# Kernel optimization log

Hardware: AMD Instinct MI355X
Metric: run time of the kernel (lower is better)

## Reference

```python
import jax, jax.numpy as jnp
import numpy as np

TOKENS, IN_F, OUT_F, R = 8192, 4096, 4096, 16
NS_STEPS = 5
NS_EPS = 1e-7


def newtonschulz5(G, steps=NS_STEPS, eps=NS_EPS):
    # Quintic Newton-Schulz orthogonalization: sigma -> 1, preserving U, V.
    a, b, c = 3.4445, -4.775, 2.0315
    X = G / (jnp.linalg.norm(G) + eps)
    transposed = G.shape[0] > G.shape[1]
    if transposed:
        X = X.T
    for _ in range(steps):
        A = X @ X.T                 # [m, m]
        B = b * A + c * (A @ A)
        X = a * X + B @ X
    if transposed:
        X = X.T
    return X


def setup_inputs() -> dict:
    key = jax.random.key(0)
    kx, kw, kb, ka, kbb = jax.random.split(key, 5)
    x = jax.random.normal(kx, (TOKENS, IN_F), dtype=jnp.float32)
    # base linear params
    W = jax.random.normal(kw, (OUT_F, IN_F), dtype=jnp.float32) / np.sqrt(IN_F)
    bias = jax.random.normal(kb, (OUT_F,), dtype=jnp.float32) * 0.01
    # LoRA params: A ~ orthogonal-ish rows, B small (init_scale/sqrt(out*r))
    lora_A = jax.random.normal(ka, (R, IN_F), dtype=jnp.float32) / np.sqrt(IN_F)
    init_std = 0.01 / np.sqrt(OUT_F * R)
    lora_B = jax.random.normal(kbb, (OUT_F, R), dtype=jnp.float32) * init_std
    return {"x": x, "W": W, "bias": bias, "lora_A": lora_A, "lora_B": lora_B}


def reference(x, W, bias, lora_A, lora_B):
    # base_out = x @ W^T + bias
    base_out = x @ W.T + bias
    # G = B A  (full [out, in] materialization, as in the original)
    G = lora_B @ lora_A
    alpha = jnp.linalg.norm(G)
    M = newtonschulz5(G)
    # lora_dropout = 0 -> identity
    lora_out = x @ M.T
    return base_out + alpha * lora_out
```

## Files before the change

### kernel.cpp

```cpp
#include <hip/hip_runtime.h>
#include <hip/hip_bf16.h>
#include <math.h>

#define TOKENS 8192
#define IN_F   4096
#define OUT_F  4096
#define LR     16

typedef __bf16 bf16_t;
typedef __attribute__((ext_vector_type(8)))  __bf16 bf16x8;
typedef __attribute__((ext_vector_type(4)))  __bf16 bf16x4;
typedef __attribute__((ext_vector_type(4)))  float  floatx4;
typedef __attribute__((ext_vector_type(16))) float  floatx16;

#define GL2LDS(gp, lp) \
    __builtin_amdgcn_global_load_lds((const __attribute__((address_space(1))) unsigned int*)(gp), \
                                     (__attribute__((address_space(3))) unsigned int*)(lp), 16, 0, 0)

__global__ void pq_kernel(const float* __restrict__ A, const float* __restrict__ B,
                          float* __restrict__ P, float* __restrict__ Q) {
    __shared__ float red[256];
    const int b = blockIdx.x, t = threadIdx.x;
    float s = 0.f;
    if (b < 256) {
        const int i = b >> 4, j = b & 15;
        const float* ai = A + (size_t)i * IN_F;
        const float* aj = A + (size_t)j * IN_F;
        for (int k = t; k < IN_F; k += 256) s += ai[k] * aj[k];
    } else {
        const int i = (b - 256) >> 4, j = (b - 256) & 15;
        for (int k = t; k < OUT_F; k += 256) s += B[k * LR + i] * B[k * LR + j];
    }
    red[t] = s; __syncthreads();
    for (int off = 128; off > 0; off >>= 1) {
        if (t < off) red[t] += red[t + off];
        __syncthreads();
    }
    if (t == 0) {
        if (b < 256) P[b] = red[0];
        else         Q[b - 256] = red[0];
    }
}

__global__ void ns_kernel(const float* __restrict__ P, const float* __restrict__ Q,
                          float* __restrict__ Sc) {
    __shared__ double Ps[256], Qs[256], Ss[256], Ys[256], Zs[256], Ts[256], Us[256], Vs[256];
    __shared__ double alpha_s, inv_n;
    const int t = threadIdx.x, i = t >> 4, j = t & 15;
    Ps[t] = P[t]; Qs[t] = Q[t];
    __syncthreads();
    if (t == 0) {
        double s = 0.0;
        for (int a = 0; a < 16; ++a)
            for (int b2 = 0; b2 < 16; ++b2) s += Ps[a * 16 + b2] * Qs[b2 * 16 + a];
        const double al = sqrt(s);
        alpha_s = al;
        inv_n   = 1.0 / (al + 1e-7);
    }
    __syncthreads();
    Ss[t] = (i == j) ? inv_n : 0.0;
    __syncthreads();
    const double ca = 3.4445, cb = -4.775, cc = 2.0315;
    for (int step = 0; step < 5; ++step) {
        double s;
        s = 0; for (int q = 0; q < 16; ++q) s += Ss[i*16+q] * Ps[q*16+j]; Ys[t] = s; __syncthreads();
        s = 0; for (int q = 0; q < 16; ++q) s += Ys[i*16+q] * Ss[j*16+q]; Zs[t] = s; __syncthreads();
        s = 0; for (int q = 0; q < 16; ++q) s += Zs[i*16+q] * Qs[q*16+j]; Ts[t] = s; __syncthreads();
        s = 0; for (int q = 0; q < 16; ++q) s += Ts[i*16+q] * Ss[q*16+j]; Us[t] = s; __syncthreads();
        s = 0; for (int q = 0; q < 16; ++q) s += Ts[i*16+q] * Us[q*16+j]; Vs[t] = s; __syncthreads();
        Ss[t] = ca * Ss[t] + cb * Us[t] + cc * Vs[t];
        __syncthreads();
    }
    Sc[t] = (float)(alpha_s * Ss[t]);
}

__global__ void sca_kernel(const float* __restrict__ Sc, const float* __restrict__ A,
                           float* __restrict__ ScA) {
    const int idx = blockIdx.x * 256 + threadIdx.x;
    const int r = idx >> 12, i = idx & 4095;
    float s = 0.f;
    for (int q = 0; q < 16; ++q) s += Sc[r * 16 + q] * A[q * IN_F + i];
    ScA[r * IN_F + i] = s;
}

__global__ void weff_kernel(const float* __restrict__ W, const float* __restrict__ Bm,
                            const float* __restrict__ ScA, bf16_t* __restrict__ Wb) {
    const int b = blockIdx.x, t = threadIdx.x;
    const int o0 = (b >> 2) * 4;
    const int i  = (b & 3) * 1024 + t * 4;
    float4 acc[4];
    #pragma unroll
    for (int r = 0; r < 4; ++r) acc[r] = *(const float4*)&W[(size_t)(o0 + r) * IN_F + i];
    #pragma unroll
    for (int q = 0; q < LR; ++q) {
        const float4 sa = *(const float4*)&ScA[q * IN_F + i];
        #pragma unroll
        for (int r = 0; r < 4; ++r) {
            const float bq = Bm[(o0 + r) * LR + q];
            acc[r].x += bq * sa.x; acc[r].y += bq * sa.y;
            acc[r].z += bq * sa.z; acc[r].w += bq * sa.w;
        }
    }
    #pragma unroll
    for (int r = 0; r < 4; ++r) {
        bf16x4 v;
        v[0] = (__bf16)acc[r].x; v[1] = (__bf16)acc[r].y;
        v[2] = (__bf16)acc[r].z; v[3] = (__bf16)acc[r].w;
        *(bf16x4*)&Wb[(size_t)(o0 + r) * IN_F + i] = v;
    }
}

__global__ void cvtx_kernel(const float* __restrict__ x, bf16_t* __restrict__ Xb) {
    const int idx = blockIdx.x * 256 + threadIdx.x;
    const float4 u = ((const float4*)x)[idx];
    bf16x4 v;
    v[0] = (__bf16)u.x; v[1] = (__bf16)u.y; v[2] = (__bf16)u.z; v[3] = (__bf16)u.w;
    ((bf16x4*)Xb)[idx] = v;
}

#define BM 128
#define BN 128
#define BK 32

__global__ __launch_bounds__(256) void gemm_kernel(
        const bf16_t* __restrict__ Xb, const bf16_t* __restrict__ Wb,
        const float* __restrict__ bias, float* __restrict__ out) {
    __shared__ bf16_t lA[BM * BK];
    __shared__ bf16_t lB[BN * BK];
    const int t = threadIdx.x;
    const int lane = t & 63, wv = t >> 6;
    const int wm = wv & 1, wn = wv >> 1;

    const int lin = blockIdx.x;
    const int st = lin >> 6, within = lin & 63;
    const int n_tile = (st & 3) * 8 + (within & 7);
    const int m_tile = (st >> 2) * 8 + (within >> 3);
    const int m0 = m_tile * BM, n0 = n_tile * BN;

    const int r0s = t >> 2, ps = t & 3;
    const int cs = (ps - ((r0s >> 1) & 3) + 4) & 3;
    const bf16_t* gA0 = Xb + (size_t)(m0 + r0s) * IN_F + cs * 8;
    const bf16_t* gA1 = gA0 + (size_t)64 * IN_F;
    const bf16_t* gB0 = Wb + (size_t)(n0 + r0s) * IN_F + cs * 8;
    const bf16_t* gB1 = gB0 + (size_t)64 * IN_F;
    bf16_t* sA0 = &lA[t * 8];        bf16_t* sA1 = &lA[(t + 256) * 8];
    bf16_t* sB0 = &lB[t * 8];        bf16_t* sB1 = &lB[(t + 256) * 8];

    const int ln = lane & 31, kg = lane >> 5;
    const int rot = (ln >> 1) & 3;
    const bf16_t* fA = &lA[(wm * 64 + ln) * BK];
    const bf16_t* fB = &lB[(wn * 64 + ln) * BK];

    floatx16 acc00 = {}, acc01 = {}, acc10 = {}, acc11 = {};

    for (int kt = 0; kt < IN_F / BK; ++kt) {
        const int ko = kt * BK;
        GL2LDS(gA0 + ko, sA0);
        GL2LDS(gA1 + ko, sA1);
        GL2LDS(gB0 + ko, sB0);
        GL2LDS(gB1 + ko, sB1);
        __syncthreads();
        #pragma unroll
        for (int s = 0; s < 2; ++s) {
            const int po = ((s * 2 + kg + rot) & 3) * 8;
            const bf16x8 a0 = *(const bf16x8*)(fA + po);
            const bf16x8 a1 = *(const bf16x8*)(fA + 32 * BK + po);
            const bf16x8 b0 = *(const bf16x8*)(fB + po);
            const bf16x8 b1 = *(const bf16x8*)(fB + 32 * BK + po);
            acc00 = __builtin_amdgcn_mfma_f32_32x32x16_bf16(a0, b0, acc00, 0, 0, 0);
            acc01 = __builtin_amdgcn_mfma_f32_32x32x16_bf16(a0, b1, acc01, 0, 0, 0);
            acc10 = __builtin_amdgcn_mfma_f32_32x32x16_bf16(a1, b0, acc10, 0, 0, 0);
            acc11 = __builtin_amdgcn_mfma_f32_32x32x16_bf16(a1, b1, acc11, 0, 0, 0);
        }
        __syncthreads();
    }

    const int colb = n0 + wn * 64 + ln;
    const int rowb = m0 + wm * 64 + 4 * kg;
    const float bv0 = bias[colb];
    const float bv1 = bias[colb + 32];
    #pragma unroll
    for (int rg = 0; rg < 16; ++rg) {
        const int row = rowb + (rg & 3) + 8 * (rg >> 2);
        out[(size_t)row * OUT_F + colb]             = acc00[rg] + bv0;
        out[(size_t)row * OUT_F + colb + 32]        = acc01[rg] + bv1;
        out[(size_t)(row + 32) * OUT_F + colb]      = acc10[rg] + bv0;
        out[(size_t)(row + 32) * OUT_F + colb + 32] = acc11[rg] + bv1;
    }
}

extern "C" void kernel_launch(void* const* d_in, const int* in_sizes, int n_in,
                              void* d_out, int out_size, void* d_ws, size_t ws_size,
                              hipStream_t stream) {
    const float* x    = (const float*)d_in[0];
    const float* W    = (const float*)d_in[1];
    const float* bias = (const float*)d_in[2];
    const float* lA_  = (const float*)d_in[3];
    const float* lB_  = (const float*)d_in[4];
    float* out = (float*)d_out;

    char* ws = (char*)d_ws;
    bf16_t* Xb  = (bf16_t*)ws;
    bf16_t* Wb  = (bf16_t*)(ws + 67108864);
    float*  ScA = (float*)(ws + 100663296);
    float*  P   = (float*)(ws + 100925440);
    float*  Q   = P + 256;
    float*  Sc  = Q + 256;

    pq_kernel  <<<512, 256, 0, stream>>>(lA_, lB_, P, Q);
    ns_kernel  <<<1, 256, 0, stream>>>(P, Q, Sc);
    sca_kernel <<<256, 256, 0, stream>>>(Sc, lA_, ScA);
    weff_kernel<<<4096, 256, 0, stream>>>(W, lB_, ScA, Wb);
    cvtx_kernel<<<TOKENS * IN_F / 4 / 256, 256, 0, stream>>>(x, Xb);
    gemm_kernel<<<2048, 256, 0, stream>>>(Xb, Wb, bias, out);
}
```

Measured before the change: 610.6 us.

## Double GEMM K-tile to 64 with 8-way swizzle and merge prep kernels

Merges the x-to-bf16 conversion and the effective-weight build into one launch, removing a kernel boundary. The GEMM K tile grows from 32 to 64, with the LDS swizzle widened to 8 chunks per row. This halves the number of loop iterations and barriers per output tile. LDS use doubles to 32 KB per block, which may lower occupancy.

```diff
diff --git a/kernel.cpp b/kernel.cpp
--- a/kernel.cpp
+++ b/kernel.cpp
@@ -83,11 +83,21 @@
     ScA[r * IN_F + i] = s;
 }
 
-__global__ void weff_kernel(const float* __restrict__ W, const float* __restrict__ Bm,
+__global__ void prep_kernel(const float* __restrict__ x, bf16_t* __restrict__ Xb,
+                            const float* __restrict__ W, const float* __restrict__ Bm,
                             const float* __restrict__ ScA, bf16_t* __restrict__ Wb) {
     const int b = blockIdx.x, t = threadIdx.x;
-    const int o0 = (b >> 2) * 4;
-    const int i  = (b & 3) * 1024 + t * 4;
+    if (b < 32768) {
+        const int idx = b * 256 + t;
+        const float4 u = ((const float4*)x)[idx];
+        bf16x4 v;
+        v[0] = (__bf16)u.x; v[1] = (__bf16)u.y; v[2] = (__bf16)u.z; v[3] = (__bf16)u.w;
+        ((bf16x4*)Xb)[idx] = v;
+        return;
+    }
+    const int bb = b - 32768;
+    const int o0 = (bb >> 2) * 4;
+    const int i  = (bb & 3) * 1024 + t * 4;
     float4 acc[4];
     #pragma unroll
     for (int r = 0; r < 4; ++r) acc[r] = *(const float4*)&W[(size_t)(o0 + r) * IN_F + i];
@@ -110,17 +120,9 @@
     }
 }
 
-__global__ void cvtx_kernel(const float* __restrict__ x, bf16_t* __restrict__ Xb) {
-    const int idx = blockIdx.x * 256 + threadIdx.x;
-    const float4 u = ((const float4*)x)[idx];
-    bf16x4 v;
-    v[0] = (__bf16)u.x; v[1] = (__bf16)u.y; v[2] = (__bf16)u.z; v[3] = (__bf16)u.w;
-    ((bf16x4*)Xb)[idx] = v;
-}
-
 #define BM 128
 #define BN 128
-#define BK 32
+#define BK 64
 
 __global__ __launch_bounds__(256) void gemm_kernel(
         const bf16_t* __restrict__ Xb, const bf16_t* __restrict__ Wb,
@@ -137,17 +139,13 @@
     const int m_tile = (st >> 2) * 8 + (within >> 3);
     const int m0 = m_tile * BM, n0 = n_tile * BN;
 
-    const int r0s = t >> 2, ps = t & 3;
-    const int cs = (ps - ((r0s >> 1) & 3) + 4) & 3;
-    const bf16_t* gA0 = Xb + (size_t)(m0 + r0s) * IN_F + cs * 8;
-    const bf16_t* gA1 = gA0 + (size_t)64 * IN_F;
-    const bf16_t* gB0 = Wb + (size_t)(n0 + r0s) * IN_F + cs * 8;
-    const bf16_t* gB1 = gB0 + (size_t)64 * IN_F;
-    bf16_t* sA0 = &lA[t * 8];        bf16_t* sA1 = &lA[(t + 256) * 8];
-    bf16_t* sB0 = &lB[t * 8];        bf16_t* sB1 = &lB[(t + 256) * 8];
+    const int rsub = t >> 3;
+    const int cs = ((t & 7) - (rsub & 7) + 8) & 7;
+    const bf16_t* gA = Xb + (size_t)(m0 + rsub) * IN_F + cs * 8;
+    const bf16_t* gB = Wb + (size_t)(n0 + rsub) * IN_F + cs * 8;
 
     const int ln = lane & 31, kg = lane >> 5;
-    const int rot = (ln >> 1) & 3;
+    const int rot = ln & 7;
     const bf16_t* fA = &lA[(wm * 64 + ln) * BK];
     const bf16_t* fB = &lB[(wn * 64 + ln) * BK];
 
@@ -155,14 +153,16 @@
 
     for (int kt = 0; kt < IN_F / BK; ++kt) {
         const int ko = kt * BK;
-        GL2LDS(gA0 + ko, sA0);
-        GL2LDS(gA1 + ko, sA1);
-        GL2LDS(gB0 + ko, sB0);
-        GL2LDS(gB1 + ko, sB1);
-        __syncthreads();
-        #pragma unroll
-        for (int s = 0; s < 2; ++s) {
-            const int po = ((s * 2 + kg + rot) & 3) * 8;
+        #pragma unroll
+        for (int j = 0; j < 4; ++j)
+            GL2LDS(gA + ko + (size_t)j * 32 * IN_F, &lA[j * 2048 + t * 8]);
+        #pragma unroll
+        for (int j = 0; j < 4; ++j)
+            GL2LDS(gB + ko + (size_t)j * 32 * IN_F, &lB[j * 2048 + t * 8]);
+        __syncthreads();
+        #pragma unroll
+        for (int s = 0; s < 4; ++s) {
+            const int po = ((s * 2 + kg + rot) & 7) * 8;
             const bf16x8 a0 = *(const bf16x8*)(fA + po);
             const bf16x8 a1 = *(const bf16x8*)(fA + 32 * BK + po);
             const bf16x8 b0 = *(const bf16x8*)(fB + po);
@@ -210,7 +210,6 @@
     pq_kernel  <<<512, 256, 0, stream>>>(lA_, lB_, P, Q);
     ns_kernel  <<<1, 256, 0, stream>>>(P, Q, Sc);
     sca_kernel <<<256, 256, 0, stream>>>(Sc, lA_, ScA);
-    weff_kernel<<<4096, 256, 0, stream>>>(W, lB_, ScA, Wb);
-    cvtx_kernel<<<TOKENS * IN_F / 4 / 256, 256, 0, stream>>>(x, Xb);
+    prep_kernel<<<36864, 256, 0, stream>>>(x, Xb, W, lB_, ScA, Wb);
     gemm_kernel<<<2048, 256, 0, stream>>>(Xb, Wb, bias, out);
 }
```

After: 576.1 us. 1.06x faster.
